# Kernel tuning notes

Measured on AMD Instinct MI355X. Metric: run time of the kernel, lower is better.

## Reference

```python
import jax, jax.numpy as jnp
import numpy as np
import math

# adaptive_schedule(t=100): t_norm=0.9 -> n_clusters~417 -> 256 -> patch_size=2, k_neighbors=16 (static)
PATCH = 2
K_NEIGH = 16
WIN = 4  # int(sqrt(k_neighbors)) neighborhood window
HID = 1152
HEADS = 16
DH = HID // HEADS
IMG = 32
GRID = IMG // PATCH  # 16 -> 256 tokens
N = GRID * GRID
IN_CH = 4
OUT_CH = 8  # learn_sigma -> 2*in_channels
B = 16
L = 2
NUM_CLASSES = 1000


def _sincos_2d(dim, gs):
    def _1d(d, pos):
        omega = 1.0 / 10000 ** (np.arange(d // 2, dtype=np.float64) / (d / 2.0))
        out = np.einsum('m,d->md', pos.reshape(-1), omega)
        return np.concatenate([np.sin(out), np.cos(out)], axis=1)
    gh = np.arange(gs, dtype=np.float32)
    gw = np.arange(gs, dtype=np.float32)
    grid = np.stack(np.meshgrid(gw, gh), axis=0).reshape(2, -1)
    return np.concatenate([_1d(dim // 2, grid[0]), _1d(dim // 2, grid[1])], axis=1)


def setup_inputs():
    key = jax.random.key(0)
    ks = iter(jax.random.split(key, 32))
    s = 0.02
    d = {}
    d['x'] = jax.random.normal(next(ks), (B, IN_CH, IMG, IMG), jnp.float32)
    d['t'] = jnp.full((B,), 100.0, jnp.float32)  # fixed timestep -> adaptive_schedule -> (2, 16)
    d['y'] = jax.random.randint(next(ks), (B,), 0, NUM_CLASSES)
    d['pos_embed'] = jnp.asarray(_sincos_2d(HID, 4), jnp.float32)[None]  # (1,16,HID) original 4x4 grid
    d['patch_w'] = s * jax.random.normal(next(ks), (HID, IN_CH, PATCH, PATCH), jnp.float32)
    d['patch_b'] = jnp.zeros((HID,), jnp.float32)
    d['t_w1'] = s * jax.random.normal(next(ks), (256, HID), jnp.float32)
    d['t_b1'] = jnp.zeros((HID,), jnp.float32)
    d['t_w2'] = s * jax.random.normal(next(ks), (HID, HID), jnp.float32)
    d['t_b2'] = jnp.zeros((HID,), jnp.float32)
    d['y_table'] = s * jax.random.normal(next(ks), (NUM_CLASSES + 1, HID), jnp.float32)
    d['ada_w'] = s * jax.random.normal(next(ks), (L, HID, 6 * HID), jnp.float32)
    d['ada_b'] = jnp.zeros((L, 6 * HID), jnp.float32)
    d['qkv_w'] = s * jax.random.normal(next(ks), (L, HID, 3 * HID), jnp.float32)
    d['qkv_b'] = jnp.zeros((L, 3 * HID), jnp.float32)
    d['proj_w'] = s * jax.random.normal(next(ks), (L, HID, HID), jnp.float32)
    d['proj_b'] = jnp.zeros((L, HID), jnp.float32)
    d['mlp_w1'] = s * jax.random.normal(next(ks), (L, HID, 4 * HID), jnp.float32)
    d['mlp_b1'] = jnp.zeros((L, 4 * HID), jnp.float32)
    d['mlp_w2'] = s * jax.random.normal(next(ks), (L, 4 * HID, HID), jnp.float32)
    d['mlp_b2'] = jnp.zeros((L, HID), jnp.float32)
    d['fl_ada_w'] = s * jax.random.normal(next(ks), (HID, 2 * HID), jnp.float32)
    d['fl_ada_b'] = jnp.zeros((2 * HID,), jnp.float32)
    d['fl_w'] = s * jax.random.normal(next(ks), (HID, PATCH * PATCH * OUT_CH), jnp.float32)
    d['fl_b'] = jnp.zeros((PATCH * PATCH * OUT_CH,), jnp.float32)
    return d


def _ln(x, eps=1e-6):
    m = jnp.mean(x, -1, keepdims=True)
    v = jnp.var(x, -1, keepdims=True)
    return (x - m) * jax.lax.rsqrt(v + eps)


def _modulate(x, shift, scale):
    return x * (1 + scale[:, None]) + shift[:, None]


def _neighborhood_attn(x, qkv_w, qkv_b, proj_w, proj_b):
    # x: (B,N,C) laid out on GRIDxGRID; each query attends to a WINxWIN (=k_neighbors) window
    # clamped at borders (NATTEN-style shifted neighborhoods), avoiding any dense NxN score matrix.
    b = x.shape[0]
    qkv = (x @ qkv_w + qkv_b).reshape(b, GRID, GRID, 3, HEADS, DH)
    q, k, v = qkv[:, :, :, 0], qkv[:, :, :, 1], qkv[:, :, :, 2]  # (B,H,W,h,d)
    starts = jnp.clip(jnp.arange(GRID) - WIN // 2, 0, GRID - WIN)
    idx = starts[:, None] + jnp.arange(WIN)[None, :]

    def gather(a):
        a = a[:, idx]
        a = a[:, :, :, idx]
        return jnp.transpose(a, (0, 1, 3, 2, 4, 5, 6))

    kn, vn = gather(k), gather(v)
    scale = DH ** -0.5
    att = jnp.einsum('bijhd,bijpqhd->bijhpq', q * scale, kn).reshape(b, GRID, GRID, HEADS, WIN * WIN)
    att = jax.nn.softmax(att, axis=-1).reshape(b, GRID, GRID, HEADS, WIN, WIN)
    out = jnp.einsum('bijhpq,bijpqhd->bijhd', att, vn).reshape(b, N, HID)
    return out @ proj_w + proj_b


def reference(x, t, y, pos_embed, patch_w, patch_b, t_w1, t_b1, t_w2, t_b2, y_table,
              ada_w, ada_b, qkv_w, qkv_b, proj_w, proj_b, mlp_w1, mlp_b1, mlp_w2, mlp_b2,
              fl_ada_w, fl_ada_b, fl_w, fl_b):
    b = x.shape[0]
    # FlexiPatchEmbed at adaptive patch size (p=2)
    h = jax.lax.conv_general_dilated(x, patch_w, (PATCH, PATCH), 'VALID',
                                     dimension_numbers=('NCHW', 'OIHW', 'NCHW'))
    h = h.reshape(b, HID, N).transpose(0, 2, 1) + patch_b
    # resize_abs_pos_embed: 4x4 -> GRIDxGRID, bicubic
    pe = jax.image.resize(pos_embed.reshape(1, 4, 4, HID), (1, GRID, GRID, HID), method='bicubic')
    h = h + pe.reshape(1, N, HID)
    # TimestepEmbedder: sinusoidal (cos|sin) -> Linear, SiLU, Linear
    half = 128
    freqs = jnp.exp(-math.log(10000.0) * jnp.arange(half, dtype=jnp.float32) / half)
    args = t[:, None] * freqs[None]
    temb = jnp.concatenate([jnp.cos(args), jnp.sin(args)], axis=-1)
    temb = jax.nn.silu(temb @ t_w1 + t_b1) @ t_w2 + t_b2
    c = temb + y_table[y]  # eval mode: no label dropout
    for l in range(L):
        mod = jax.nn.silu(c) @ ada_w[l] + ada_b[l]
        sh1, sc1, g1, sh2, sc2, g2 = jnp.split(mod, 6, axis=-1)
        h = h + g1[:, None] * _neighborhood_attn(_modulate(_ln(h), sh1, sc1),
                                                 qkv_w[l], qkv_b[l], proj_w[l], proj_b[l])
        z = _modulate(_ln(h), sh2, sc2)
        z = jax.nn.gelu(z @ mlp_w1[l] + mlp_b1[l], approximate=True) @ mlp_w2[l] + mlp_b2[l]
        h = h + g2[:, None] * z
    # final_layer_ps_2 + unpatchify
    sh, sc = jnp.split(jax.nn.silu(c) @ fl_ada_w + fl_ada_b, 2, axis=-1)
    h = _modulate(_ln(h), sh, sc) @ fl_w + fl_b  # (B,N,p*p*OUT_CH)
    h = h.reshape(b, GRID, GRID, PATCH, PATCH, OUT_CH)
    return jnp.einsum('bhwpqc->bchpwq', h).reshape(b, OUT_CH, IMG, IMG)
```

## Files before the change

kernel.cpp:

```cpp
#include <hip/hip_runtime.h>
#include <cmath>

static constexpr int kHid = 1152;
static constexpr int kM   = 4096;

typedef __bf16 bf16x8 __attribute__((ext_vector_type(8)));
typedef float  f32x4  __attribute__((ext_vector_type(4)));

struct BicW { float w[16][4]; };

__device__ __forceinline__ float dev_silu(float x) { return x / (1.0f + expf(-x)); }
__device__ __forceinline__ float dev_gelu(float x) {
  float u = 0.7978845608028654f * (x + 0.044715f * x * x * x);
  return 0.5f * x * (1.0f + tanhf(u));
}

__device__ __forceinline__ void glds16(const void* g, void* l) {
  __builtin_amdgcn_global_load_lds(
      (const __attribute__((address_space(1))) unsigned int*)g,
      (__attribute__((address_space(3))) unsigned int*)l, 16, 0, 0);
}

__global__ __launch_bounds__(256) void k_patch_pos(
    const float* __restrict__ x, const float* __restrict__ pw,
    const float* __restrict__ pb, const float* __restrict__ pos,
    float* __restrict__ h, BicW W)
{
  const int total = kM * kHid;
  for (int idx = blockIdx.x * blockDim.x + threadIdx.x; idx < total;
       idx += gridDim.x * blockDim.x) {
    int c  = idx % kHid;
    int t  = idx / kHid;
    int b  = t >> 8;
    int gy = (t >> 4) & 15;
    int gx = t & 15;
    float acc = pb[c];
    const float* xb  = x + (size_t)b * 4 * 1024;
    const float* pwc = pw + (size_t)c * 16;
#pragma unroll
    for (int ic = 0; ic < 4; ic++)
#pragma unroll
      for (int p = 0; p < 2; p++)
#pragma unroll
        for (int q = 0; q < 2; q++)
          acc += xb[ic * 1024 + (gy * 2 + p) * 32 + gx * 2 + q] *
                 pwc[(ic * 2 + p) * 2 + q];
    float pe = 0.f;
#pragma unroll
    for (int iy = 0; iy < 4; iy++) {
      float ra = 0.f;
#pragma unroll
      for (int ix = 0; ix < 4; ix++)
        ra += W.w[gx][ix] * pos[(iy * 4 + ix) * kHid + c];
      pe += W.w[gy][iy] * ra;
    }
    h[idx] = acc + pe;
  }
}

__global__ __launch_bounds__(256) void k_temb1(
    const float* __restrict__ t, const float* __restrict__ w1,
    const float* __restrict__ b1, float* __restrict__ hid1)
{
  int b  = blockIdx.y;
  int j0 = blockIdx.x * 64;
  int tid = threadIdx.x;
  __shared__ float e[256];
  if (tid < 128) {
    float fr  = expf(-9.210340371976184f * (float)tid / 128.0f);
    float arg = t[b] * fr;
    e[tid]       = cosf(arg);
    e[tid + 128] = sinf(arg);
  }
  __syncthreads();
  int j = tid & 63, ks = tid >> 6;
  float acc = 0.f;
#pragma unroll 4
  for (int k = ks * 64; k < ks * 64 + 64; k++)
    acc += e[k] * w1[k * kHid + j0 + j];
  __shared__ float part[4][64];
  part[ks][j] = acc;
  __syncthreads();
  if (ks == 0) {
    float v = part[0][j] + part[1][j] + part[2][j] + part[3][j] + b1[j0 + j];
    hid1[b * kHid + j0 + j] = dev_silu(v);
  }
}

__global__ __launch_bounds__(256) void k_temb2(
    const float* __restrict__ hid1, const float* __restrict__ w2,
    const float* __restrict__ b2, const float* __restrict__ ytab,
    const int* __restrict__ y, float* __restrict__ c, float* __restrict__ sc)
{
  int b  = blockIdx.y;
  int j0 = blockIdx.x * 64;
  __shared__ float hs[kHid];
  for (int k = threadIdx.x; k < kHid; k += 256) hs[k] = hid1[b * kHid + k];
  __syncthreads();
  int j = threadIdx.x & 63, ks = threadIdx.x >> 6;
  float acc = 0.f;
#pragma unroll 4
  for (int k = ks * 288; k < ks * 288 + 288; k++)
    acc += hs[k] * w2[(size_t)k * kHid + j0 + j];
  __shared__ float part[4][64];
  part[ks][j] = acc;
  __syncthreads();
  if (ks == 0) {
    int jj = j0 + j;
    float v = part[0][j] + part[1][j] + part[2][j] + part[3][j] + b2[jj] +
              ytab[(size_t)y[b] * kHid + jj];
    c[b * kHid + jj]  = v;
    sc[b * kHid + jj] = dev_silu(v);
  }
}

__global__ __launch_bounds__(256) void k_ada(
    const float* __restrict__ scb, const float* __restrict__ w,
    const float* __restrict__ bias, float* __restrict__ out, int Nout)
{
  int b  = blockIdx.y;
  int j0 = blockIdx.x * 64;
  __shared__ float cs[kHid];
  for (int k = threadIdx.x; k < kHid; k += 256) cs[k] = scb[b * kHid + k];
  __syncthreads();
  int j = threadIdx.x & 63, ks = threadIdx.x >> 6;
  float acc = 0.f;
#pragma unroll 4
  for (int k = ks * 288; k < ks * 288 + 288; k++)
    acc += cs[k] * w[(size_t)k * Nout + j0 + j];
  __shared__ float part[4][64];
  part[ks][j] = acc;
  __syncthreads();
  if (ks == 0)
    out[(size_t)b * Nout + j0 + j] =
        part[0][j] + part[1][j] + part[2][j] + part[3][j] + bias[j0 + j];
}

struct ConvDesc { const float* src; __bf16* dst; int K, N, tilesX; int start; };
struct ConvDescs { ConvDesc d[4]; };

__global__ __launch_bounds__(256) void k_convw4(ConvDescs cd)
{
  int bid = blockIdx.x;
  int e = 0;
#pragma unroll
  for (int i = 1; i < 4; i++) if (bid >= cd.d[i].start) e = i;
  const ConvDesc& D = cd.d[e];
  int lid = bid - D.start;
  int tx = lid % D.tilesX, ty = lid / D.tilesX;
  int n0 = tx * 32, k0 = ty * 32;
  __shared__ float tile[32][33];
  int c = threadIdx.x & 31, r = threadIdx.x >> 5;
#pragma unroll
  for (int i = 0; i < 32; i += 8)
    tile[r + i][c] = D.src[(size_t)(k0 + r + i) * D.N + n0 + c];
  __syncthreads();
#pragma unroll
  for (int i = 0; i < 32; i += 8) {
    int nn = r + i;
    D.dst[(size_t)(n0 + nn) * D.K + k0 + c] = (__bf16)tile[c][nn];
  }
}

__global__ __launch_bounds__(256) void k_ln_mod(
    const float* __restrict__ h, const float* __restrict__ mod, int mstride,
    int sh_off, int sc_off, __bf16* __restrict__ out)
{
  int token = blockIdx.x;
  int b = token >> 8;
  const float* x = h + (size_t)token * kHid;
  float s = 0.f, ss = 0.f;
  for (int c = threadIdx.x; c < kHid; c += 256) {
    float v = x[c]; s += v; ss += v * v;
  }
#pragma unroll
  for (int o = 32; o > 0; o >>= 1) {
    s += __shfl_down(s, o, 64); ss += __shfl_down(ss, o, 64);
  }
  __shared__ float red[2][4];
  __shared__ float stats[2];
  int wave = threadIdx.x >> 6, lane = threadIdx.x & 63;
  if (lane == 0) { red[0][wave] = s; red[1][wave] = ss; }
  __syncthreads();
  if (threadIdx.x == 0) {
    float S  = red[0][0] + red[0][1] + red[0][2] + red[0][3];
    float SS = red[1][0] + red[1][1] + red[1][2] + red[1][3];
    float mean = S * (1.0f / kHid);
    float var  = SS * (1.0f / kHid) - mean * mean;
    stats[0] = mean;
    stats[1] = rsqrtf(var + 1e-6f);
  }
  __syncthreads();
  float mean = stats[0], rstd = stats[1];
  const float* shv = mod + (size_t)b * mstride + sh_off;
  const float* scv = mod + (size_t)b * mstride + sc_off;
  __bf16* o = out + (size_t)token * kHid;
  for (int c = threadIdx.x; c < kHid; c += 256) {
    float v = (x[c] - mean) * rstd;
    o[c] = (__bf16)(v * (1.f + scv[c]) + shv[c]);
  }
}

template<int RB, int CB, int MODE, typename OutT>
__global__ __launch_bounds__(256) void mfma_gemm(
    const __bf16* __restrict__ A, const __bf16* __restrict__ Wt,
    const float* __restrict__ bias, OutT* C,
    const float* __restrict__ gate, int gstride,
    int Kslice, int Ktot, int Nout)
{
  constexpr int BM = RB * 32;
  constexpr int BN = CB * 32;
  __shared__ __attribute__((aligned(16))) __bf16 As[BM * 32];
  __shared__ __attribute__((aligned(16))) __bf16 Bs[BN * 32];

  const int tid  = threadIdx.x;
  const int lane = tid & 63;
  const int wv   = tid >> 6;
  const int wy   = wv >> 1, wx = wv & 1;
  const int l15  = lane & 15;
  const int quad = lane >> 4;
  const int m0   = blockIdx.y * BM;
  const int n0   = blockIdx.x * BN;
  const int kbase = blockIdx.z * Kslice;

  f32x4 acc[RB][CB] = {};

  const int arow0 = tid >> 2;
  const int akc   = (tid & 3) * 8;

  for (int k0 = kbase; k0 < kbase + Kslice; k0 += 32) {
#pragma unroll
    for (int p = 0; p < BM / 64; p++) {
      int row = arow0 + p * 64;
      glds16(A + (size_t)(m0 + row) * Ktot + k0 + akc, &As[(row * 32) + akc]);
    }
#pragma unroll
    for (int p = 0; p < BN / 64; p++) {
      int row = arow0 + p * 64;
      glds16(Wt + (size_t)(n0 + row) * Ktot + k0 + akc, &Bs[(row * 32) + akc]);
    }
    __syncthreads();

    bf16x8 af[RB], bf[CB];
#pragma unroll
    for (int r = 0; r < RB; r++)
      af[r] = *(const bf16x8*)&As[(wy * RB * 16 + r * 16 + l15) * 32 + quad * 8];
#pragma unroll
    for (int c2 = 0; c2 < CB; c2++)
      bf[c2] = *(const bf16x8*)&Bs[(wx * CB * 16 + c2 * 16 + l15) * 32 + quad * 8];
#pragma unroll
    for (int r = 0; r < RB; r++)
#pragma unroll
      for (int c2 = 0; c2 < CB; c2++)
        acc[r][c2] = __builtin_amdgcn_mfma_f32_16x16x32_bf16(af[r], bf[c2], acc[r][c2], 0, 0, 0);
    __syncthreads();
  }

  const int bidx = m0 >> 8;
  const bool addb = (blockIdx.z == 0);
#pragma unroll
  for (int c2 = 0; c2 < CB; c2++) {
    int col = n0 + wx * CB * 16 + c2 * 16 + l15;
    float bcol = addb ? bias[col] : 0.f;
    float gv = (MODE == 2) ? gate[(size_t)bidx * gstride + col] : 0.f;
#pragma unroll
    for (int r = 0; r < RB; r++) {
      int mbase = m0 + wy * RB * 16 + r * 16 + quad * 4;
#pragma unroll
      for (int reg = 0; reg < 4; reg++) {
        float v = acc[r][c2][reg] + bcol;
        size_t off = (size_t)(mbase + reg) * Nout + col;
        if (MODE == 0) C[off] = (OutT)v;
        if (MODE == 1) C[off] = (OutT)dev_gelu(v);
        if (MODE == 2) unsafeAtomicAdd((float*)&C[off], gv * v);
      }
    }
  }
}

__global__ __launch_bounds__(256) void k_attn(const __bf16* __restrict__ qkv,
                                              __bf16* __restrict__ out)
{
  int token = blockIdx.x;
  int b = token >> 8;
  int i = (token >> 4) & 15;
  int j = token & 15;
  int si = min(max(i - 2, 0), 12);
  int sj = min(max(j - 2, 0), 12);
  __shared__ float att[16][17];
  __shared__ float prob[16][17];

  int hh = threadIdx.x >> 4;
  int pq = threadIdx.x & 15;
  int ni = si + (pq >> 2);
  int nj = sj + (pq & 3);
  int ntok = (b << 8) | (ni << 4) | nj;
  const __bf16* qp = qkv + (size_t)token * 3456 + hh * 72;
  const __bf16* kp = qkv + (size_t)ntok  * 3456 + kHid + hh * 72;
  float s = 0.f;
#pragma unroll
  for (int dc = 0; dc < 9; dc++) {
    bf16x8 qv = *(const bf16x8*)(qp + dc * 8);
    bf16x8 kv = *(const bf16x8*)(kp + dc * 8);
#pragma unroll
    for (int d = 0; d < 8; d++) s += (float)qv[d] * (float)kv[d];
  }
  att[hh][pq] = s * 0.11785113019775793f;
  __syncthreads();
  if (threadIdx.x < 16) {
    int hd = threadIdx.x;
    float m = att[hd][0];
    for (int e2 = 1; e2 < 16; e2++) m = fmaxf(m, att[hd][e2]);
    float sum = 0.f;
    for (int e2 = 0; e2 < 16; e2++) {
      float ex = expf(att[hd][e2] - m);
      prob[hd][e2] = ex;
      sum += ex;
    }
    float inv = 1.f / sum;
    for (int e2 = 0; e2 < 16; e2++) prob[hd][e2] *= inv;
  }
  __syncthreads();
  if (threadIdx.x < 144) {
    int hd = threadIdx.x / 9;
    int dc = threadIdx.x - hd * 9;
    float a8[8] = {};
#pragma unroll
    for (int e2 = 0; e2 < 16; e2++) {
      int nt = (b << 8) | ((si + (e2 >> 2)) << 4) | (sj + (e2 & 3));
      bf16x8 vv = *(const bf16x8*)(qkv + (size_t)nt * 3456 + 2304 + hd * 72 + dc * 8);
      float p = prob[hd][e2];
#pragma unroll
      for (int d = 0; d < 8; d++) a8[d] += p * (float)vv[d];
    }
    bf16x8 ov;
#pragma unroll
    for (int d = 0; d < 8; d++) ov[d] = (__bf16)a8[d];
    *(bf16x8*)(out + (size_t)token * kHid + hd * 72 + dc * 8) = ov;
  }
}

__global__ __launch_bounds__(256) void k_final(
    const float* __restrict__ h, const float* __restrict__ flm,
    const float* __restrict__ fw, const float* __restrict__ fb,
    float* __restrict__ out)
{
  int token = blockIdx.x;
  int b = token >> 8;
  const float* x = h + (size_t)token * kHid;
  float s = 0.f, ss = 0.f;
  for (int c = threadIdx.x; c < kHid; c += 256) { float v = x[c]; s += v; ss += v * v; }
#pragma unroll
  for (int o = 32; o > 0; o >>= 1) {
    s += __shfl_down(s, o, 64); ss += __shfl_down(ss, o, 64);
  }
  __shared__ float red[2][4];
  __shared__ float stats[2];
  __shared__ float xs[kHid];
  int wave = threadIdx.x >> 6, lane = threadIdx.x & 63;
  if (lane == 0) { red[0][wave] = s; red[1][wave] = ss; }
  __syncthreads();
  if (threadIdx.x == 0) {
    float S  = red[0][0] + red[0][1] + red[0][2] + red[0][3];
    float SS = red[1][0] + red[1][1] + red[1][2] + red[1][3];
    float mean = S * (1.0f / kHid);
    float var  = SS * (1.0f / kHid) - mean * mean;
    stats[0] = mean; stats[1] = rsqrtf(var + 1e-6f);
  }
  __syncthreads();
  float mean = stats[0], rstd = stats[1];
  const float* shv = flm + (size_t)b * 2304;
  const float* scv = shv + kHid;
  for (int c = threadIdx.x; c < kHid; c += 256)
    xs[c] = ((x[c] - mean) * rstd) * (1.f + scv[c]) + shv[c];
  __syncthreads();
  if (threadIdx.x < 32) {
    int jj = threadIdx.x;
    float acc = fb[jj];
    for (int k = 0; k < kHid; k++) acc += xs[k] * fw[k * 32 + jj];
    int p = jj >> 4, q = (jj >> 3) & 1, cc = jj & 7;
    int gy = (token >> 4) & 15, gx = token & 15;
    out[(((size_t)b * 8 + cc) * 32 + (gy * 2 + p)) * 32 + (gx * 2 + q)] = acc;
  }
}

extern "C" void kernel_launch(void* const* d_in, const int* in_sizes, int n_in,
                              void* d_out, int out_size, void* d_ws, size_t ws_size,
                              hipStream_t stream)
{
  const float* x        = (const float*)d_in[0];
  const float* t        = (const float*)d_in[1];
  const int*   y        = (const int*)  d_in[2];
  const float* pos      = (const float*)d_in[3];
  const float* patch_w  = (const float*)d_in[4];
  const float* patch_b  = (const float*)d_in[5];
  const float* t_w1     = (const float*)d_in[6];
  const float* t_b1     = (const float*)d_in[7];
  const float* t_w2     = (const float*)d_in[8];
  const float* t_b2     = (const float*)d_in[9];
  const float* y_table  = (const float*)d_in[10];
  const float* ada_w    = (const float*)d_in[11];
  const float* ada_b    = (const float*)d_in[12];
  const float* qkv_w    = (const float*)d_in[13];
  const float* qkv_b    = (const float*)d_in[14];
  const float* proj_w   = (const float*)d_in[15];
  const float* proj_b   = (const float*)d_in[16];
  const float* mlp_w1   = (const float*)d_in[17];
  const float* mlp_b1   = (const float*)d_in[18];
  const float* mlp_w2   = (const float*)d_in[19];
  const float* mlp_b2   = (const float*)d_in[20];
  const float* fl_ada_w = (const float*)d_in[21];
  const float* fl_ada_b = (const float*)d_in[22];
  const float* fl_w     = (const float*)d_in[23];
  const float* fl_b     = (const float*)d_in[24];
  float* out = (float*)d_out;

  float* ws   = (float*)d_ws;
  float*  h    = ws;
  __bf16* xmod = (__bf16*)(h + (size_t)4096 * 1152);
  __bf16* big  = xmod + (size_t)4096 * 1152;
  __bf16* wq   = big  + (size_t)4096 * 4608;
  __bf16* wp   = wq   + (size_t)3456 * 1152;
  __bf16* wm1  = wp   + (size_t)1152 * 1152;
  __bf16* wm2  = wm1  + (size_t)4608 * 1152;
  float*  cbuf = (float*)(wm2 + (size_t)1152 * 4608);
  float*  scb  = cbuf + 16 * 1152;
  float*  hid1 = scb  + 16 * 1152;
  float*  mod  = hid1 + 16 * 1152;
  float*  flm  = mod  + 16 * 6912;

  BicW W;
  for (int o = 0; o < 16; o++) {
    double sf = (o + 0.5) * 0.25 - 0.5;
    double wd[4]; double tot = 0.0;
    const double a = -0.5;
    for (int i = 0; i < 4; i++) {
      double d = fabs(sf - (double)i);
      double v;
      if (d <= 1.0)      v = ((a + 2.0) * d - (a + 3.0)) * d * d + 1.0;
      else if (d < 2.0)  v = a * (((d - 5.0) * d + 8.0) * d - 4.0);
      else               v = 0.0;
      wd[i] = v; tot += v;
    }
    for (int i = 0; i < 4; i++) W.w[o][i] = (float)(wd[i] / tot);
  }

  k_patch_pos<<<4608, 256, 0, stream>>>(x, patch_w, patch_b, pos, h, W);
  k_temb1<<<dim3(18, 16), 256, 0, stream>>>(t, t_w1, t_b1, hid1);
  k_temb2<<<dim3(18, 16), 256, 0, stream>>>(hid1, t_w2, t_b2, y_table, y, cbuf, scb);

  for (int l = 0; l < 2; l++) {
    ConvDescs cd;
    cd.d[0] = { qkv_w  + (size_t)l * 1152 * 3456, wq,  1152, 3456, 108, 0 };
    cd.d[1] = { proj_w + (size_t)l * 1152 * 1152, wp,  1152, 1152,  36, 3888 };
    cd.d[2] = { mlp_w1 + (size_t)l * 1152 * 4608, wm1, 1152, 4608, 144, 3888 + 1296 };
    cd.d[3] = { mlp_w2 + (size_t)l * 4608 * 1152, wm2, 4608, 1152,  36, 3888 + 1296 + 5184 };
    k_convw4<<<3888 + 1296 + 5184 + 5184, 256, 0, stream>>>(cd);

    const float* ab = ada_b + (size_t)l * 6912;
    k_ada<<<dim3(108, 16), 256, 0, stream>>>(scb, ada_w + (size_t)l * 1152 * 6912, ab, mod, 6912);

    k_ln_mod<<<4096, 256, 0, stream>>>(h, mod, 6912, 0, 1152, xmod);
    mfma_gemm<4, 4, 0, __bf16><<<dim3(27, 32), 256, 0, stream>>>(
        xmod, wq, qkv_b + (size_t)l * 3456, big, nullptr, 0, 1152, 1152, 3456);
    k_attn<<<4096, 256, 0, stream>>>(big, xmod);
    mfma_gemm<4, 2, 2, float><<<dim3(18, 32, 2), 256, 0, stream>>>(
        xmod, wp, proj_b + (size_t)l * 1152, h, mod + 2304, 6912, 576, 1152, 1152);

    k_ln_mod<<<4096, 256, 0, stream>>>(h, mod, 6912, 3456, 4608, xmod);
    mfma_gemm<4, 4, 1, __bf16><<<dim3(36, 32), 256, 0, stream>>>(
        xmod, wm1, mlp_b1 + (size_t)l * 4608, big, nullptr, 0, 1152, 1152, 4608);
    mfma_gemm<4, 2, 2, float><<<dim3(18, 32, 2), 256, 0, stream>>>(
        big, wm2, mlp_b2 + (size_t)l * 1152, h, mod + 5760, 6912, 2304, 4608, 1152);
  }

  k_ada<<<dim3(36, 16), 256, 0, stream>>>(scb, fl_ada_w, fl_ada_b, flm, 2304);
  k_final<<<4096, 256, 0, stream>>>(h, flm, fl_w, fl_b, out);
}
```

Before: 1.240 ms.

## Use 64-wide K tiles with XOR-swizzled LDS and drop split-K atomics

The GEMM K step grows from 32 to 64, so each barrier pair now covers two MFMA sub-steps. LDS rows are written and read through an XOR swizzle of the 16-byte chunk index to avoid bank conflicts on the wider rows. Split-K on the proj and MLP-down GEMMs is removed, so the gated residual becomes a plain read-modify-write instead of a float atomic. This halves the grid for those two GEMMs, which may lower occupancy, and doubles LDS use per block.

```diff
diff --git a/kernel.cpp b/kernel.cpp
--- a/kernel.cpp
+++ b/kernel.cpp
@@ -205,13 +205,12 @@
 __global__ __launch_bounds__(256) void mfma_gemm(
     const __bf16* __restrict__ A, const __bf16* __restrict__ Wt,
     const float* __restrict__ bias, OutT* C,
-    const float* __restrict__ gate, int gstride,
-    int Kslice, int Ktot, int Nout)
+    const float* __restrict__ gate, int gstride, int K, int Nout)
 {
   constexpr int BM = RB * 32;
   constexpr int BN = CB * 32;
-  __shared__ __attribute__((aligned(16))) __bf16 As[BM * 32];
-  __shared__ __attribute__((aligned(16))) __bf16 Bs[BN * 32];
+  __shared__ __attribute__((aligned(16))) __bf16 As[BM * 64];
+  __shared__ __attribute__((aligned(16))) __bf16 Bs[BN * 64];
 
   const int tid  = threadIdx.x;
   const int lane = tid & 63;
@@ -221,47 +220,50 @@
   const int quad = lane >> 4;
   const int m0   = blockIdx.y * BM;
   const int n0   = blockIdx.x * BN;
-  const int kbase = blockIdx.z * Kslice;
 
   f32x4 acc[RB][CB] = {};
 
-  const int arow0 = tid >> 2;
-  const int akc   = (tid & 3) * 8;
-
-  for (int k0 = kbase; k0 < kbase + Kslice; k0 += 32) {
-#pragma unroll
-    for (int p = 0; p < BM / 64; p++) {
-      int row = arow0 + p * 64;
-      glds16(A + (size_t)(m0 + row) * Ktot + k0 + akc, &As[(row * 32) + akc]);
-    }
-#pragma unroll
-    for (int p = 0; p < BN / 64; p++) {
-      int row = arow0 + p * 64;
-      glds16(Wt + (size_t)(n0 + row) * Ktot + k0 + akc, &Bs[(row * 32) + akc]);
+  const int lrow = lane >> 3;
+  const int cpos = lane & 7;
+  const int gk   = (cpos ^ lrow) * 8;
+
+  for (int k0 = 0; k0 < K; k0 += 64) {
+#pragma unroll
+    for (int p = 0; p < BM / 32; p++) {
+      int row = p * 32 + wv * 8 + lrow;
+      glds16(A + (size_t)(m0 + row) * K + k0 + gk, &As[row * 64 + cpos * 8]);
+    }
+#pragma unroll
+    for (int p = 0; p < BN / 32; p++) {
+      int row = p * 32 + wv * 8 + lrow;
+      glds16(Wt + (size_t)(n0 + row) * K + k0 + gk, &Bs[row * 64 + cpos * 8]);
     }
     __syncthreads();
 
-    bf16x8 af[RB], bf[CB];
-#pragma unroll
-    for (int r = 0; r < RB; r++)
-      af[r] = *(const bf16x8*)&As[(wy * RB * 16 + r * 16 + l15) * 32 + quad * 8];
-#pragma unroll
-    for (int c2 = 0; c2 < CB; c2++)
-      bf[c2] = *(const bf16x8*)&Bs[(wx * CB * 16 + c2 * 16 + l15) * 32 + quad * 8];
-#pragma unroll
-    for (int r = 0; r < RB; r++)
+#pragma unroll
+    for (int ks = 0; ks < 2; ks++) {
+      const int perm = ((ks * 4 + quad) ^ (l15 & 7)) * 8;
+      bf16x8 af[RB], bf[CB];
+#pragma unroll
+      for (int r = 0; r < RB; r++)
+        af[r] = *(const bf16x8*)&As[(wy * RB * 16 + r * 16 + l15) * 64 + perm];
 #pragma unroll
       for (int c2 = 0; c2 < CB; c2++)
-        acc[r][c2] = __builtin_amdgcn_mfma_f32_16x16x32_bf16(af[r], bf[c2], acc[r][c2], 0, 0, 0);
+        bf[c2] = *(const bf16x8*)&Bs[(wx * CB * 16 + c2 * 16 + l15) * 64 + perm];
+#pragma unroll
+      for (int r = 0; r < RB; r++)
+#pragma unroll
+        for (int c2 = 0; c2 < CB; c2++)
+          acc[r][c2] = __builtin_amdgcn_mfma_f32_16x16x32_bf16(af[r], bf[c2], acc[r][c2], 0, 0, 0);
+    }
     __syncthreads();
   }
 
   const int bidx = m0 >> 8;
-  const bool addb = (blockIdx.z == 0);
 #pragma unroll
   for (int c2 = 0; c2 < CB; c2++) {
     int col = n0 + wx * CB * 16 + c2 * 16 + l15;
-    float bcol = addb ? bias[col] : 0.f;
+    float bcol = bias[col];
     float gv = (MODE == 2) ? gate[(size_t)bidx * gstride + col] : 0.f;
 #pragma unroll
     for (int r = 0; r < RB; r++) {
@@ -272,7 +274,7 @@
         size_t off = (size_t)(mbase + reg) * Nout + col;
         if (MODE == 0) C[off] = (OutT)v;
         if (MODE == 1) C[off] = (OutT)dev_gelu(v);
-        if (MODE == 2) unsafeAtomicAdd((float*)&C[off], gv * v);
+        if (MODE == 2) C[off] = C[off] + (OutT)(gv * v);
       }
     }
   }
@@ -462,16 +464,16 @@
 
     k_ln_mod<<<4096, 256, 0, stream>>>(h, mod, 6912, 0, 1152, xmod);
     mfma_gemm<4, 4, 0, __bf16><<<dim3(27, 32), 256, 0, stream>>>(
-        xmod, wq, qkv_b + (size_t)l * 3456, big, nullptr, 0, 1152, 1152, 3456);
+        xmod, wq, qkv_b + (size_t)l * 3456, big, nullptr, 0, 1152, 3456);
     k_attn<<<4096, 256, 0, stream>>>(big, xmod);
-    mfma_gemm<4, 2, 2, float><<<dim3(18, 32, 2), 256, 0, stream>>>(
-        xmod, wp, proj_b + (size_t)l * 1152, h, mod + 2304, 6912, 576, 1152, 1152);
+    mfma_gemm<4, 2, 2, float><<<dim3(18, 32), 256, 0, stream>>>(
+        xmod, wp, proj_b + (size_t)l * 1152, h, mod + 2304, 6912, 1152, 1152);
 
     k_ln_mod<<<4096, 256, 0, stream>>>(h, mod, 6912, 3456, 4608, xmod);
     mfma_gemm<4, 4, 1, __bf16><<<dim3(36, 32), 256, 0, stream>>>(
-        xmod, wm1, mlp_b1 + (size_t)l * 4608, big, nullptr, 0, 1152, 1152, 4608);
-    mfma_gemm<4, 2, 2, float><<<dim3(18, 32, 2), 256, 0, stream>>>(
-        big, wm2, mlp_b2 + (size_t)l * 1152, h, mod + 5760, 6912, 2304, 4608, 1152);
+        xmod, wm1, mlp_b1 + (size_t)l * 4608, big, nullptr, 0, 1152, 4608);
+    mfma_gemm<4, 2, 2, float><<<dim3(18, 32), 256, 0, stream>>>(
+        big, wm2, mlp_b2 + (size_t)l * 1152, h, mod + 5760, 6912, 4608, 1152);
   }
 
   k_ada<<<dim3(36, 16), 256, 0, stream>>>(scb, fl_ada_w, fl_ada_b, flm, 2304);
```

Result: faster. 1.053 ms (-15.1%).
